# Kernel optimization log

Measured on AMD Instinct MI355X. Metric: run time of the kernel, lower is better.

The kernel has to match this reference:

```python
import jax, jax.numpy as jnp
import numpy as np
from jax import lax

# Quantized ConvBnA block: int8 conv with int32 accumulation, per-channel
# bias add (folded BN), power-of-two requant via arithmetic right shift,
# clamp, and narrow-int cast (uint8 since Act_min >= 0 -> pure_positive).

N, CIN, COUT, H, W, K = 32, 128, 256, 56, 56, 3

def setup_inputs() -> dict:
    key = jax.random.key(0)
    k1, k2, k3 = jax.random.split(key, 3)
    # int8-valued inputs / weights (stored as int32 per harness dtype support)
    x = jax.random.randint(k1, (N, CIN, H, W), -64, 64, dtype=jnp.int32)
    weight = jax.random.randint(k2, (COUT, CIN, K, K), -128, 128, dtype=jnp.int32)
    # BN_shift is negative (shift right by -n = 8 bits)
    n = jnp.full((1, COUT, 1, 1), -8, dtype=jnp.int32)
    # folded-BN integer bias, broadcasts over [N, C, H, W]
    t = jax.random.randint(k3, (1, COUT, 1, 1), -2048, 2048, dtype=jnp.int32)
    act_min = 0
    act_max = 255
    return {"x": x, "weight": weight, "n": n, "t": t,
            "act_min": act_min, "act_max": act_max}

def reference(x, weight, n, t, act_min, act_max):
    # int32-accumulated convolution (stride 1, pad 1, dilation 1, groups 1)
    acc = lax.conv_general_dilated(
        x.astype(jnp.int32), weight.astype(jnp.int32),
        window_strides=(1, 1), padding=((1, 1), (1, 1)),
        dimension_numbers=("NCHW", "OIHW", "NCHW"))
    acc = acc + t                              # folded-BN bias add
    acc = jnp.right_shift(acc, -n)             # pow2 requant, arithmetic shift
    acc = jnp.clip(acc, jnp.int32(act_min), jnp.int32(act_max))
    # pure_positive (Act_min >= 0) -> small unsigned type
    return acc.astype(jnp.uint8)
```

## Files before the change

kernel.cpp:

```cpp
#include <hip/hip_runtime.h>
#include <cstdint>


typedef __attribute__((ext_vector_type(4))) int i32x4;
typedef __attribute__((ext_vector_type(2))) int i32x2;

#define C_IN   128
#define C_OUT  256
#define HW2    3136
#define OUT_NSTRIDE 802816

#define XQ_BYTES 12845056
#define WQ_OFF   XQ_BYTES
#define WQ_BYTES 294912
#define ZP_OFF   (WQ_OFF + WQ_BYTES)

__device__ __forceinline__ void gload_lds16(const void* g, void* l) {
  __builtin_amdgcn_global_load_lds(
      (const __attribute__((address_space(1))) void*)(uintptr_t)g,
      (__attribute__((address_space(3))) void*)(uint32_t)(uintptr_t)l,
      16, 0, 0);
}

__global__ void wxform(const int* __restrict__ w, char* __restrict__ wq,
                       int* __restrict__ zp) {
  int id = blockIdx.x * 256 + threadIdx.x;
  int ci = id & 127;
  int co = (id >> 7) & 255;
  int g  = id >> 15;
  wq[id] = (char)w[co * 1152 + ci * 9 + g];
  if (blockIdx.x == 0 && threadIdx.x < 64) zp[threadIdx.x] = 0;
}

__global__ __launch_bounds__(256) void xform(const int* __restrict__ x,
                                             char* __restrict__ xq) {
  int bid = blockIdx.x;
  int hb = bid % 49;
  int n  = bid / 49;
  int t  = threadIdx.x;
  int cig = t & 15;
  int hw0 = (t >> 4) * 4;
  const int* src = x + n * (C_IN * HW2) + hb * 64 + hw0;
  i32x4 ld[8];
#pragma unroll
  for (int j = 0; j < 8; j++)
    ld[j] = *(const i32x4*)(src + (cig * 8 + j) * HW2);
  char* dst = xq + (size_t)(n * HW2 + hb * 64 + hw0) * 128 + cig * 8;
#pragma unroll
  for (int p = 0; p < 4; p++) {
    unsigned lo = (ld[0][p] & 255) | ((ld[1][p] & 255) << 8) |
                  ((ld[2][p] & 255) << 16) | ((unsigned)(ld[3][p] & 255) << 24);
    unsigned hi = (ld[4][p] & 255) | ((ld[5][p] & 255) << 8) |
                  ((ld[6][p] & 255) << 16) | ((unsigned)(ld[7][p] & 255) << 24);
    i32x2 v; v[0] = (int)lo; v[1] = (int)hi;
    *(i32x2*)(dst + p * 128) = v;
  }
}

__global__ __launch_bounds__(256, 2) void conv_mfma(
    const char* __restrict__ xq, const char* __restrict__ wq,
    const char* __restrict__ zp,
    const int* __restrict__ nshift, const int* __restrict__ tbias,
    const int* __restrict__ aminp, const int* __restrict__ amaxp,
    int* __restrict__ out) {
  __shared__ char lds[65536];

  const int tid = threadIdx.x;
  const int bid = blockIdx.x;
  const int bm = bid & 1;
  const int pb = bid >> 1;
  const int l  = tid & 63;
  const int wid = tid >> 6;
  const int wm = wid >> 1, wn = wid & 1;

  const int chl = tid & 7;
  const int rsw = (tid >> 3) & 7;
  const int chg = chl ^ rsw;
  const int kboff = chg * 16;

  int p_idx[4], p_h[4], p_w[4];
#pragma unroll
  for (int i = 0; i < 4; i++) {
    int pr = (tid >> 3) + i * 32;
    int p  = pb * 128 + pr;
    int n  = p / HW2;
    int hw = p - n * HW2;
    int h  = hw / 56;
    int w  = hw - h * 56;
    p_idx[i] = p; p_h[i] = h; p_w[i] = w;
  }

  auto stageAB = [&](int g, int buf) {
    char* Ab = lds + buf * 32768;
    char* Bb = Ab + 16384;
    const int dh = g / 3 - 1, dw = g % 3 - 1;
    const int doff = dh * 56 + dw;
    const char* wsrc = wq + (((g * 256 + bm * 128)) << 7) + kboff;
#pragma unroll
    for (int i = 0; i < 4; i++) {
      int row = (tid >> 3) + i * 32;
      gload_lds16(wsrc + (row << 7), Ab + (tid + i * 256) * 16);
    }
#pragma unroll
    for (int i = 0; i < 4; i++) {
      int h2 = p_h[i] + dh, w2 = p_w[i] + dw;
      bool valid = ((unsigned)h2 < 56u) && ((unsigned)w2 < 56u);
      const char* gp = valid ? (xq + ((size_t)(p_idx[i] + doff) << 7) + kboff)
                             : zp;
      gload_lds16(gp, Bb + (tid + i * 256) * 16);
    }
  };

  i32x4 acc[4][4] = {};
  const int lrow = l & 15;
  const int lk   = (l >> 4) * 16;
  const int lsw  = (l & 7) << 4;

  auto computeStep = [&](int buf) {
    char* Ab = lds + buf * 32768;
    char* Bb = Ab + 16384;
#pragma unroll
    for (int kk = 0; kk < 2; kk++) {
      i32x4 a[4], b[4];
      const int cb = ((kk * 64 + lk) ^ lsw);
#pragma unroll
      for (int mi = 0; mi < 4; mi++) {
        int row = wm * 64 + mi * 16 + lrow;
        a[mi] = *(const i32x4*)(Ab + (row << 7) + cb);
      }
#pragma unroll
      for (int ni = 0; ni < 4; ni++) {
        int row = wn * 64 + ni * 16 + lrow;
        b[ni] = *(const i32x4*)(Bb + (row << 7) + cb);
      }
#pragma unroll
      for (int mi = 0; mi < 4; mi++)
#pragma unroll
        for (int ni = 0; ni < 4; ni++)
          acc[mi][ni] = __builtin_amdgcn_mfma_i32_16x16x64_i8(
              a[mi], b[ni], acc[mi][ni], 0, 0, 0);
    }
  };

  stageAB(0, 0);
#pragma unroll 1
  for (int s = 0; s < 9; ++s) {
    const int s1 = s + 1;
    if (s1 < 9) stageAB(s1, s1 & 1);
    __builtin_amdgcn_sched_barrier(0);
    if (s1 < 9) { asm volatile("s_waitcnt vmcnt(8)" ::: "memory"); }
    else        { asm volatile("s_waitcnt vmcnt(0)" ::: "memory"); }
    __builtin_amdgcn_s_barrier();
    __builtin_amdgcn_sched_barrier(0);
    computeStep(s & 1);
    __builtin_amdgcn_sched_barrier(0);
    __builtin_amdgcn_s_barrier();
    __builtin_amdgcn_sched_barrier(0);
  }

  const int amin = aminp[0], amax = amaxp[0];
  int pbase[4];
#pragma unroll
  for (int ni = 0; ni < 4; ni++) {
    int p = pb * 128 + wn * 64 + ni * 16 + lrow;
    int n = p / HW2;
    int hw = p - n * HW2;
    pbase[ni] = n * OUT_NSTRIDE + hw;
  }
#pragma unroll
  for (int mi = 0; mi < 4; mi++) {
    int co0 = bm * 128 + wm * 64 + mi * 16 + ((l >> 4) << 2);
    const int4 t4 = *(const int4*)(tbias + co0);
    const int4 n4 = *(const int4*)(nshift + co0);
#pragma unroll
    for (int ni = 0; ni < 4; ni++) {
#pragma unroll
      for (int r = 0; r < 4; r++) {
        int tv = (r == 0) ? t4.x : (r == 1) ? t4.y : (r == 2) ? t4.z : t4.w;
        int nv = (r == 0) ? n4.x : (r == 1) ? n4.y : (r == 2) ? n4.z : n4.w;
        int v = acc[mi][ni][r] + tv;
        v = v >> (-nv);
        v = v < amin ? amin : (v > amax ? amax : v);
        out[pbase[ni] + (co0 + r) * HW2] = v;
      }
    }
  }
}

extern "C" void kernel_launch(void* const* d_in, const int* in_sizes, int n_in,
                              void* d_out, int out_size, void* d_ws, size_t ws_size,
                              hipStream_t stream) {
  const int* x      = (const int*)d_in[0];
  const int* w      = (const int*)d_in[1];
  const int* nshift = (const int*)d_in[2];
  const int* tbias  = (const int*)d_in[3];
  const int* aminp  = (const int*)d_in[4];
  const int* amaxp  = (const int*)d_in[5];
  int* out = (int*)d_out;

  char* xq = (char*)d_ws;
  char* wq = (char*)d_ws + WQ_OFF;
  char* zp = (char*)d_ws + ZP_OFF;

  hipLaunchKernelGGL(wxform, dim3(1152), dim3(256), 0, stream, w, wq, (int*)zp);
  hipLaunchKernelGGL(xform,  dim3(1568), dim3(256), 0, stream, x, xq);
  hipLaunchKernelGGL(conv_mfma, dim3(1568), dim3(256), 0, stream,
                     xq, wq, zp, nshift, tbias, aminp, amaxp, out);
}
```

Baseline: 186.0 us.

## Restructure conv MFMA kernel: 512 threads, triple-buffered LDS, chunk-major layout, block swizzle

The conv kernel moves from 256 to 512 threads per block, with 8 waves each owning a 64x32 tile instead of 4 waves owning 64x64. The LDS buffer grows to three 32KB stages so loads run two taps ahead, and each tap's loads are spread across the two k-halves of compute. The LDS layout changes from XOR-swizzled row-major to chunk-major, and s_setprio is raised around MFMA bursts. A block-index swizzle groups blocks that share weights, aiming at better L2 reuse. The cost is lower occupancy (one block per CU) and extra barriers per k-step.

After: 215.6 us. +15.9%, slower.

```diff
diff --git a/kernel.cpp b/kernel.cpp
--- a/kernel.cpp
+++ b/kernel.cpp
@@ -6,7 +6,6 @@
 typedef __attribute__((ext_vector_type(2))) int i32x2;
 
 #define C_IN   128
-#define C_OUT  256
 #define HW2    3136
 #define OUT_NSTRIDE 802816
 
@@ -57,115 +56,105 @@
   }
 }
 
-__global__ __launch_bounds__(256, 2) void conv_mfma(
+__global__ __launch_bounds__(512, 1) void conv_mfma(
     const char* __restrict__ xq, const char* __restrict__ wq,
     const char* __restrict__ zp,
     const int* __restrict__ nshift, const int* __restrict__ tbias,
     const int* __restrict__ aminp, const int* __restrict__ amaxp,
     int* __restrict__ out) {
-  __shared__ char lds[65536];
+  __shared__ char lds[98304];
 
   const int tid = threadIdx.x;
   const int bid = blockIdx.x;
-  const int bm = bid & 1;
-  const int pb = bid >> 1;
-  const int l  = tid & 63;
+  const int swz = (bid & 7) * 196 + (bid >> 3);
+  const int bm = swz / 784;
+  const int pb = swz % 784;
+  const int l   = tid & 63;
   const int wid = tid >> 6;
-  const int wm = wid >> 1, wn = wid & 1;
+  const int wm = wid >> 2;
+  const int wn = wid & 3;
 
-  const int chl = tid & 7;
-  const int rsw = (tid >> 3) & 7;
-  const int chg = chl ^ rsw;
-  const int kboff = chg * 16;
+  const int r_ = tid & 127;
+  const int c0 = tid >> 7;
+  const char* wsrcA = wq + (bm * 128 + r_) * 128;
+  const int p = pb * 128 + r_;
+  const int n_img = p / HW2;
+  const int hw = p - n_img * HW2;
+  const int ph = hw / 56, pw = hw - (hw / 56) * 56;
+  const char* xsrc = xq + (size_t)p * 128;
 
-  int p_idx[4], p_h[4], p_w[4];
-#pragma unroll
-  for (int i = 0; i < 4; i++) {
-    int pr = (tid >> 3) + i * 32;
-    int p  = pb * 128 + pr;
-    int n  = p / HW2;
-    int hw = p - n * HW2;
-    int h  = hw / 56;
-    int w  = hw - h * 56;
-    p_idx[i] = p; p_h[i] = h; p_w[i] = w;
-  }
-
-  auto stageAB = [&](int g, int buf) {
-    char* Ab = lds + buf * 32768;
-    char* Bb = Ab + 16384;
-    const int dh = g / 3 - 1, dw = g % 3 - 1;
-    const int doff = dh * 56 + dw;
-    const char* wsrc = wq + (((g * 256 + bm * 128)) << 7) + kboff;
-#pragma unroll
-    for (int i = 0; i < 4; i++) {
-      int row = (tid >> 3) + i * 32;
-      gload_lds16(wsrc + (row << 7), Ab + (tid + i * 256) * 16);
-    }
-#pragma unroll
-    for (int i = 0; i < 4; i++) {
-      int h2 = p_h[i] + dh, w2 = p_w[i] + dw;
-      bool valid = ((unsigned)h2 < 56u) && ((unsigned)w2 < 56u);
-      const char* gp = valid ? (xq + ((size_t)(p_idx[i] + doff) << 7) + kboff)
-                             : zp;
-      gload_lds16(gp, Bb + (tid + i * 256) * 16);
-    }
+  auto stageA = [&](int g, char* Ab) {
+    const char* s = wsrcA + g * 32768;
+    gload_lds16(s + c0 * 16,       Ab + (c0 * 128 + r_) * 16);
+    gload_lds16(s + (c0 + 4) * 16, Ab + ((c0 + 4) * 128 + r_) * 16);
+  };
+  auto stageB = [&](int g, char* Bb) {
+    const int g3 = g / 3;
+    const int dh = g3 - 1, dw = g - g3 * 3 - 1;
+    const bool valid = ((unsigned)(ph + dh) < 56u) && ((unsigned)(pw + dw) < 56u);
+    const char* s = valid ? (xsrc + (dh * 56 + dw) * 128) : zp;
+    gload_lds16(s + c0 * 16,       Bb + (c0 * 128 + r_) * 16);
+    gload_lds16(s + (c0 + 4) * 16, Bb + ((c0 + 4) * 128 + r_) * 16);
   };
 
-  i32x4 acc[4][4] = {};
-  const int lrow = l & 15;
-  const int lk   = (l >> 4) * 16;
-  const int lsw  = (l & 7) << 4;
+  i32x4 acc[4][2] = {};
+  const int lrow16 = (l & 15) * 16;
+  const int lch = l >> 4;
 
-  auto computeStep = [&](int buf) {
-    char* Ab = lds + buf * 32768;
+  stageA(0, lds);            stageB(0, lds + 16384);
+  stageA(1, lds + 32768);    stageB(1, lds + 32768 + 16384);
+
+  int cur = 0;
+#pragma unroll 1
+  for (int t = 0; t < 9; ++t) {
+    if (t < 8) { asm volatile("s_waitcnt vmcnt(4)" ::: "memory"); }
+    else       { asm volatile("s_waitcnt vmcnt(0)" ::: "memory"); }
+    __builtin_amdgcn_s_barrier();
+
+    char* Ab = lds + cur * 32768;
     char* Bb = Ab + 16384;
+    int nxt = cur + 2; if (nxt >= 3) nxt -= 3;
+    char* An = lds + nxt * 32768;
+
 #pragma unroll
-    for (int kk = 0; kk < 2; kk++) {
-      i32x4 a[4], b[4];
-      const int cb = ((kk * 64 + lk) ^ lsw);
+    for (int kk = 0; kk < 2; ++kk) {
+      i32x4 a[4], b[2];
+      const int coff = (kk * 4 + lch) * 2048;
 #pragma unroll
-      for (int mi = 0; mi < 4; mi++) {
-        int row = wm * 64 + mi * 16 + lrow;
-        a[mi] = *(const i32x4*)(Ab + (row << 7) + cb);
+      for (int mi = 0; mi < 4; mi++)
+        a[mi] = *(const i32x4*)(Ab + coff + wm * 1024 + mi * 256 + lrow16);
+#pragma unroll
+      for (int ni = 0; ni < 2; ni++)
+        b[ni] = *(const i32x4*)(Bb + coff + wn * 512 + ni * 256 + lrow16);
+      if (t < 7) {
+        if (kk == 0) stageA(t + 2, An);
+        else         stageB(t + 2, An + 16384);
       }
-#pragma unroll
-      for (int ni = 0; ni < 4; ni++) {
-        int row = wn * 64 + ni * 16 + lrow;
-        b[ni] = *(const i32x4*)(Bb + (row << 7) + cb);
-      }
+      __builtin_amdgcn_s_barrier();
+      asm volatile("s_waitcnt lgkmcnt(0)" ::: "memory");
+      __builtin_amdgcn_sched_barrier(0);
+      __builtin_amdgcn_s_setprio(1);
 #pragma unroll
       for (int mi = 0; mi < 4; mi++)
 #pragma unroll
-        for (int ni = 0; ni < 4; ni++)
+        for (int ni = 0; ni < 2; ni++)
           acc[mi][ni] = __builtin_amdgcn_mfma_i32_16x16x64_i8(
               a[mi], b[ni], acc[mi][ni], 0, 0, 0);
+      __builtin_amdgcn_s_setprio(0);
+      __builtin_amdgcn_sched_barrier(0);
+      __builtin_amdgcn_s_barrier();
     }
-  };
-
-  stageAB(0, 0);
-#pragma unroll 1
-  for (int s = 0; s < 9; ++s) {
-    const int s1 = s + 1;
-    if (s1 < 9) stageAB(s1, s1 & 1);
-    __builtin_amdgcn_sched_barrier(0);
-    if (s1 < 9) { asm volatile("s_waitcnt vmcnt(8)" ::: "memory"); }
-    else        { asm volatile("s_waitcnt vmcnt(0)" ::: "memory"); }
-    __builtin_amdgcn_s_barrier();
-    __builtin_amdgcn_sched_barrier(0);
-    computeStep(s & 1);
-    __builtin_amdgcn_sched_barrier(0);
-    __builtin_amdgcn_s_barrier();
-    __builtin_amdgcn_sched_barrier(0);
+    cur = cur + 1; if (cur == 3) cur = 0;
   }
 
   const int amin = aminp[0], amax = amaxp[0];
-  int pbase[4];
+  int pbase[2];
 #pragma unroll
-  for (int ni = 0; ni < 4; ni++) {
-    int p = pb * 128 + wn * 64 + ni * 16 + lrow;
-    int n = p / HW2;
-    int hw = p - n * HW2;
-    pbase[ni] = n * OUT_NSTRIDE + hw;
+  for (int ni = 0; ni < 2; ni++) {
+    int pp = pb * 128 + wn * 32 + ni * 16 + (l & 15);
+    int nn = pp / HW2;
+    int hh = pp - nn * HW2;
+    pbase[ni] = nn * OUT_NSTRIDE + hh;
   }
 #pragma unroll
   for (int mi = 0; mi < 4; mi++) {
@@ -173,7 +162,7 @@
     const int4 t4 = *(const int4*)(tbias + co0);
     const int4 n4 = *(const int4*)(nshift + co0);
 #pragma unroll
-    for (int ni = 0; ni < 4; ni++) {
+    for (int ni = 0; ni < 2; ni++) {
 #pragma unroll
       for (int r = 0; r < 4; r++) {
         int tv = (r == 0) ? t4.x : (r == 1) ? t4.y : (r == 2) ? t4.z : t4.w;
@@ -204,6 +193,6 @@
 
   hipLaunchKernelGGL(wxform, dim3(1152), dim3(256), 0, stream, w, wq, (int*)zp);
   hipLaunchKernelGGL(xform,  dim3(1568), dim3(256), 0, stream, x, xq);
-  hipLaunchKernelGGL(conv_mfma, dim3(1568), dim3(256), 0, stream,
+  hipLaunchKernelGGL(conv_mfma, dim3(1568), dim3(512), 0, stream,
                      xq, wq, zp, nshift, tbias, aminp, amaxp, out);
 }
```
